# Kernel tuning notes

Measured on AMD Instinct MI355X. Metric: run time of the kernel, lower is better.

## Reference

```python
import jax, jax.numpy as jnp
import numpy as np

TEMP = 0.07
EPS = 1e-6

B = 8192
D1 = 129  # d+1 ambient Lorentz coords


def setup_inputs() -> dict:
    key = jax.random.key(0)
    k1, k2 = jax.random.split(key)
    z1 = jax.random.normal(k1, (B, D1), dtype=jnp.float32)
    z2 = jax.random.normal(k2, (B, D1), dtype=jnp.float32)
    return {"z1": z1, "z2": z2}


def _loss(z1, z2):
    # Minkowski (Lorentz) inner product via a single GEMM:
    # <x,y>_L = -x0*y0 + sum_i xi*yi  ->  x @ (metric * y)^T
    metric = jnp.concatenate([-jnp.ones((1,), z1.dtype), jnp.ones((D1 - 1,), z1.dtype)])
    inner = jnp.einsum('bd,kd->bk', z1, z2 * metric)  # (B, B)
    # Lorentz distance with curvature c=1: acosh(clamp(-<x,y>_L, 1+eps))
    dist = jnp.arccosh(jnp.clip(-inner, 1.0 + EPS, None))
    sims = -dist / TEMP
    # symmetric InfoNCE: labels are the diagonal
    logp_t2i = jax.nn.log_softmax(sims, axis=-1)      # text -> image
    logp_i2t = jax.nn.log_softmax(sims.T, axis=-1)    # image -> text
    diag = jnp.arange(sims.shape[0])
    loss_t2i = -jnp.mean(logp_t2i[diag, diag])
    loss_i2t = -jnp.mean(logp_i2t[diag, diag])
    return (loss_t2i + loss_i2t) / 2.0


def reference(z1, z2):
    return _loss(z1, z2)
```

## Files before the change

### kernel.cpp

```cpp
#include <hip/hip_runtime.h>
#include <math.h>


#define BDIM   8192
#define K_IN   129
#define K_PAD  160
#define BK     32
#define NKT    (K_PAD / BK)
#define CTILES 4

typedef __bf16  bf16x8 __attribute__((ext_vector_type(8)));
typedef float   f32x4  __attribute__((ext_vector_type(4)));

#define OFF_A    0u
#define OFF_B    (BDIM * K_PAD * 2u)
#define OFF_RS   (2u * BDIM * K_PAD * 2u)
#define OFF_CP   (OFF_RS + BDIM * 4u)
#define OFF_DG   (OFF_CP + 4u * BDIM * 4u)

__device__ __forceinline__ float fast_sqrt(float x) {
#if __has_builtin(__builtin_amdgcn_sqrtf)
    return __builtin_amdgcn_sqrtf(x);
#else
    return sqrtf(x);
#endif
}
__device__ __forceinline__ float fast_log2(float x) {
#if __has_builtin(__builtin_amdgcn_logf)
    return __builtin_amdgcn_logf(x);
#else
    return __log2f(x);
#endif
}
__device__ __forceinline__ float fast_exp2(float x) {
#if __has_builtin(__builtin_amdgcn_exp2f)
    return __builtin_amdgcn_exp2f(x);
#else
    extern "C" __device__ float __ocml_native_exp2_f32(float);
    return __ocml_native_exp2_f32(x);
#endif
}

__device__ __forceinline__ unsigned short f2bf_rne(float f) {
    unsigned int u = __float_as_uint(f);
    u += 0x7FFFu + ((u >> 16) & 1u);
    return (unsigned short)(u >> 16);
}

__global__ __launch_bounds__(256) void convert_kernel(
    const float* __restrict__ z1, const float* __restrict__ z2,
    unsigned short* __restrict__ A, unsigned short* __restrict__ B,
    float* __restrict__ rs_cp)
{
    int idx = blockIdx.x * 256 + threadIdx.x;
    if (idx < 5 * BDIM) rs_cp[idx] = 0.f;
    if (idx >= BDIM * K_PAD) return;
    int r = idx / K_PAD;
    int c = idx - r * K_PAD;
    float va = 0.f, vb = 0.f;
    if (c < K_IN) {
        va = z1[r * K_IN + c];
        vb = z2[r * K_IN + c];
        if (c == 0) va = -va;
    }
    A[idx] = f2bf_rne(va);
    B[idx] = f2bf_rne(vb);
}

__global__ __launch_bounds__(256, 2) void gemm_epilogue_kernel(
    const unsigned short* __restrict__ A, const unsigned short* __restrict__ B,
    float* __restrict__ row_sum, float* __restrict__ col_part,
    float* __restrict__ diag)
{
    const int t    = threadIdx.x;
    const int lane = t & 63;
    const int wave = t >> 6;
    const int quad = lane >> 4;
    const int l16  = lane & 15;

    const int strip = blockIdx.x & 63;
    const int chunk = blockIdx.x >> 6;
    const int wr      = (wave >> 1) * 64;
    const int rowBase = strip * 128 + wr;
    const int colWave = chunk * 512 + (wave & 1) * 256;

    const unsigned short* Abase = A + (rowBase + l16) * K_PAD + quad * 8;
    float* colRep = col_part + (strip & 3) * BDIM;

    float rowp[4][4] = {};

    for (int ct = 0; ct < CTILES; ++ct) {
        const int colBase = colWave + ct * 64;
        const unsigned short* Bbase = B + (colBase + l16) * K_PAD + quad * 8;

        f32x4 acc[4][4] = {};
        #pragma unroll
        for (int kt = 0; kt < NKT; ++kt) {
            bf16x8 af[4], bfr[4];
            #pragma unroll
            for (int i = 0; i < 4; ++i) {
                af[i]  = *(const bf16x8*)(Abase + i * 16 * K_PAD + kt * BK);
                bfr[i] = *(const bf16x8*)(Bbase + i * 16 * K_PAD + kt * BK);
            }
            #pragma unroll
            for (int i = 0; i < 4; ++i)
                #pragma unroll
                for (int j = 0; j < 4; ++j)
                    acc[i][j] = __builtin_amdgcn_mfma_f32_16x16x32_bf16(
                                    af[i], bfr[j], acc[i][j], 0, 0, 0);
        }

        const bool diagTile = (colBase == rowBase);
        float colp[4] = {0.f, 0.f, 0.f, 0.f};

        #pragma unroll
        for (int i = 0; i < 4; ++i) {
            #pragma unroll
            for (int j = 0; j < 4; ++j) {
                #pragma unroll
                for (int reg = 0; reg < 4; ++reg) {
                    float inner = acc[i][j][reg];
                    float x = fmaxf(-inner, 1.000001f);
                    float s = fast_sqrt(__builtin_fmaf(x, x, -1.0f));
                    float l2u = fast_log2(x + s);
                    float e = fast_exp2(-14.285714285714286f * l2u);
                    rowp[i][reg] += e;
                    colp[j]      += e;
                    if (diagTile && i == j && (quad * 4 + reg) == l16) {
                        int R = rowBase + i * 16 + quad * 4 + reg;
                        diag[R] = -9.902102579427789f * l2u;
                    }
                }
            }
        }

        #pragma unroll
        for (int j = 0; j < 4; ++j) {
            float v = colp[j];
            v += __shfl_xor(v, 16);
            v += __shfl_xor(v, 32);
            if (quad == 0)
                atomicAdd(&colRep[colBase + j * 16 + l16], v);
        }
    }

    #pragma unroll
    for (int i = 0; i < 4; ++i) {
        #pragma unroll
        for (int reg = 0; reg < 4; ++reg) {
            float v = rowp[i][reg];
            v += __shfl_xor(v, 1);
            v += __shfl_xor(v, 2);
            v += __shfl_xor(v, 4);
            v += __shfl_xor(v, 8);
            if (l16 == 0)
                atomicAdd(&row_sum[rowBase + i * 16 + quad * 4 + reg], v);
        }
    }
}

__global__ __launch_bounds__(1024) void finalize_kernel(
    const float* __restrict__ rs, const float* __restrict__ cp,
    const float* __restrict__ dg, float* __restrict__ out)
{
    __shared__ float part[16];
    int t = threadIdx.x;
    float a = 0.f;
    const float LN2_HALF = 0.34657359027997264f;
    for (int b = t; b < BDIM; b += 1024) {
        float cs = cp[b] + cp[b + BDIM] + cp[b + 2 * BDIM] + cp[b + 3 * BDIM];
        a += LN2_HALF * (fast_log2(rs[b]) + fast_log2(cs)) - dg[b];
    }
    #pragma unroll
    for (int m = 1; m < 64; m <<= 1) a += __shfl_xor(a, m);
    if ((t & 63) == 0) part[t >> 6] = a;
    __syncthreads();
    if (t < 16) {
        float v = part[t];
        #pragma unroll
        for (int m = 1; m < 16; m <<= 1) v += __shfl_xor(v, m);
        if (t == 0) out[0] = v * (1.0f / (float)BDIM);
    }
}

extern "C" void kernel_launch(void* const* d_in, const int* in_sizes, int n_in,
                              void* d_out, int out_size, void* d_ws, size_t ws_size,
                              hipStream_t stream)
{
    const float* z1 = (const float*)d_in[0];
    const float* z2 = (const float*)d_in[1];
    float* out = (float*)d_out;

    char* ws = (char*)d_ws;
    unsigned short* A  = (unsigned short*)(ws + OFF_A);
    unsigned short* B  = (unsigned short*)(ws + OFF_B);
    float* row_sum     = (float*)(ws + OFF_RS);
    float* col_part    = (float*)(ws + OFF_CP);
    float* diag        = (float*)(ws + OFF_DG);

    convert_kernel<<<(BDIM * K_PAD + 255) / 256, 256, 0, stream>>>(
        z1, z2, A, B, row_sum );

    gemm_epilogue_kernel<<<1024, 256, 0, stream>>>(
        A, B, row_sum, col_part, diag);

    finalize_kernel<<<1, 1024, 0, stream>>>(row_sum, col_part, diag, out);
}
```

Measured before the change: 119.2 us.

## Software-pipeline GEMM loads, fuse finalize via last-block counter, vectorize convert

The GEMM loop is flattened across column tiles and k-steps, with a three-slot register buffer that issues operand loads two steps ahead so memory latency overlaps the MFMAs. The separate finalize kernel is removed: each block bumps a global counter, and the last block to finish reads the row, column and diagonal sums with atomic loads and writes the loss. The convert kernel now handles four elements per thread with vector stores, and it also zeroes the diagonal buffer and the counter. The costs are higher register pressure from the prefetch buffers and correctness that relies on the waitcnt-plus-counter ordering between blocks.

```diff
diff --git a/kernel.cpp b/kernel.cpp
--- a/kernel.cpp
+++ b/kernel.cpp
@@ -8,6 +8,9 @@
 #define BK     32
 #define NKT    (K_PAD / BK)
 #define CTILES 4
+#define NSTEP  (CTILES * NKT)
+#define NBLK   1024
+#define KQ     (K_PAD / 4)
 
 typedef __bf16  bf16x8 __attribute__((ext_vector_type(8)));
 typedef float   f32x4  __attribute__((ext_vector_type(4)));
@@ -17,6 +20,7 @@
 #define OFF_RS   (2u * BDIM * K_PAD * 2u)
 #define OFF_CP   (OFF_RS + BDIM * 4u)
 #define OFF_DG   (OFF_CP + 4u * BDIM * 4u)
+#define OFF_CNT  (OFF_DG + BDIM * 4u)
 
 __device__ __forceinline__ float fast_sqrt(float x) {
 #if __has_builtin(__builtin_amdgcn_sqrtf)
@@ -50,27 +54,39 @@
 __global__ __launch_bounds__(256) void convert_kernel(
     const float* __restrict__ z1, const float* __restrict__ z2,
     unsigned short* __restrict__ A, unsigned short* __restrict__ B,
-    float* __restrict__ rs_cp)
+    float* __restrict__ zero6, unsigned int* __restrict__ cnt)
 {
     int idx = blockIdx.x * 256 + threadIdx.x;
-    if (idx < 5 * BDIM) rs_cp[idx] = 0.f;
-    if (idx >= BDIM * K_PAD) return;
-    int r = idx / K_PAD;
-    int c = idx - r * K_PAD;
-    float va = 0.f, vb = 0.f;
-    if (c < K_IN) {
-        va = z1[r * K_IN + c];
-        vb = z2[r * K_IN + c];
-        if (c == 0) va = -va;
-    }
-    A[idx] = f2bf_rne(va);
-    B[idx] = f2bf_rne(vb);
+    if (idx == 0) *cnt = 0u;
+    if (idx < 6 * BDIM) zero6[idx] = 0.f;
+    if (idx >= BDIM * KQ) return;
+    int r = idx / KQ;
+    int k = (idx - r * KQ) * 4;
+    float va[4], vb[4];
+    #pragma unroll
+    for (int u = 0; u < 4; ++u) {
+        int c = k + u;
+        va[u] = 0.f; vb[u] = 0.f;
+        if (c < K_IN) {
+            va[u] = z1[r * K_IN + c];
+            vb[u] = z2[r * K_IN + c];
+            if (c == 0) va[u] = -va[u];
+        }
+    }
+    ushort4 ha, hb;
+    ha.x = f2bf_rne(va[0]); ha.y = f2bf_rne(va[1]);
+    ha.z = f2bf_rne(va[2]); ha.w = f2bf_rne(va[3]);
+    hb.x = f2bf_rne(vb[0]); hb.y = f2bf_rne(vb[1]);
+    hb.z = f2bf_rne(vb[2]); hb.w = f2bf_rne(vb[3]);
+    *(ushort4*)&A[r * K_PAD + k] = ha;
+    *(ushort4*)&B[r * K_PAD + k] = hb;
 }
 
 __global__ __launch_bounds__(256, 2) void gemm_epilogue_kernel(
     const unsigned short* __restrict__ A, const unsigned short* __restrict__ B,
     float* __restrict__ row_sum, float* __restrict__ col_part,
-    float* __restrict__ diag)
+    float* __restrict__ diag, unsigned int* __restrict__ cnt,
+    float* __restrict__ out)
 {
     const int t    = threadIdx.x;
     const int lane = t & 63;
@@ -84,63 +100,81 @@
     const int rowBase = strip * 128 + wr;
     const int colWave = chunk * 512 + (wave & 1) * 256;
 
-    const unsigned short* Abase = A + (rowBase + l16) * K_PAD + quad * 8;
+    const unsigned short* Ab = A + (rowBase + l16) * K_PAD + quad * 8;
+    const unsigned short* Bb = B + (colWave + l16) * K_PAD + quad * 8;
     float* colRep = col_part + (strip & 3) * BDIM;
 
     float rowp[4][4] = {};
-
-    for (int ct = 0; ct < CTILES; ++ct) {
-        const int colBase = colWave + ct * 64;
-        const unsigned short* Bbase = B + (colBase + l16) * K_PAD + quad * 8;
-
-        f32x4 acc[4][4] = {};
-        #pragma unroll
-        for (int kt = 0; kt < NKT; ++kt) {
-            bf16x8 af[4], bfr[4];
+    f32x4 acc[4][4] = {};
+    bf16x8 afb[3][4], bfb[3][4];
+
+    #pragma unroll
+    for (int s = 0; s < 2; ++s) {
+        const int ct = s / NKT, kt = s % NKT;
+        #pragma unroll
+        for (int i = 0; i < 4; ++i) {
+            afb[s][i] = *(const bf16x8*)(Ab + i * 16 * K_PAD + kt * BK);
+            bfb[s][i] = *(const bf16x8*)(Bb + (ct * 64 + i * 16) * K_PAD + kt * BK);
+        }
+    }
+
+    #pragma unroll
+    for (int s = 0; s < NSTEP; ++s) {
+        if (s + 2 < NSTEP) {
+            const int s2 = s + 2, ct2 = s2 / NKT, kt2 = s2 % NKT, sl2 = s2 % 3;
             #pragma unroll
             for (int i = 0; i < 4; ++i) {
-                af[i]  = *(const bf16x8*)(Abase + i * 16 * K_PAD + kt * BK);
-                bfr[i] = *(const bf16x8*)(Bbase + i * 16 * K_PAD + kt * BK);
+                afb[sl2][i] = *(const bf16x8*)(Ab + i * 16 * K_PAD + kt2 * BK);
+                bfb[sl2][i] = *(const bf16x8*)(Bb + (ct2 * 64 + i * 16) * K_PAD + kt2 * BK);
+            }
+        }
+        const int slot = s % 3;
+        #pragma unroll
+        for (int i = 0; i < 4; ++i)
+            #pragma unroll
+            for (int j = 0; j < 4; ++j)
+                acc[i][j] = __builtin_amdgcn_mfma_f32_16x16x32_bf16(
+                                afb[slot][i], bfb[slot][j], acc[i][j], 0, 0, 0);
+
+        if (s % NKT == NKT - 1) {
+            const int ct = s / NKT;
+            const int colBase = colWave + ct * 64;
+            const bool diagTile = (colBase == rowBase);
+            float colp[4] = {0.f, 0.f, 0.f, 0.f};
+
+            #pragma unroll
+            for (int i = 0; i < 4; ++i) {
+                #pragma unroll
+                for (int j = 0; j < 4; ++j) {
+                    #pragma unroll
+                    for (int reg = 0; reg < 4; ++reg) {
+                        float inner = acc[i][j][reg];
+                        float x = fmaxf(-inner, 1.000001f);
+                        float sq = fast_sqrt(__builtin_fmaf(x, x, -1.0f));
+                        float l2u = fast_log2(x + sq);
+                        float e = fast_exp2(-14.285714285714286f * l2u);
+                        rowp[i][reg] += e;
+                        colp[j]      += e;
+                        if (diagTile && i == j && (quad * 4 + reg) == l16) {
+                            int R = rowBase + i * 16 + quad * 4 + reg;
+                            atomicAdd(&diag[R], -9.902102579427789f * l2u);
+                        }
+                    }
+                }
+            }
+            #pragma unroll
+            for (int j = 0; j < 4; ++j) {
+                float v = colp[j];
+                v += __shfl_xor(v, 16);
+                v += __shfl_xor(v, 32);
+                if (quad == 0)
+                    atomicAdd(&colRep[colBase + j * 16 + l16], v);
             }
             #pragma unroll
             for (int i = 0; i < 4; ++i)
                 #pragma unroll
                 for (int j = 0; j < 4; ++j)
-                    acc[i][j] = __builtin_amdgcn_mfma_f32_16x16x32_bf16(
-                                    af[i], bfr[j], acc[i][j], 0, 0, 0);
-        }
-
-        const bool diagTile = (colBase == rowBase);
-        float colp[4] = {0.f, 0.f, 0.f, 0.f};
-
-        #pragma unroll
-        for (int i = 0; i < 4; ++i) {
-            #pragma unroll
-            for (int j = 0; j < 4; ++j) {
-                #pragma unroll
-                for (int reg = 0; reg < 4; ++reg) {
-                    float inner = acc[i][j][reg];
-                    float x = fmaxf(-inner, 1.000001f);
-                    float s = fast_sqrt(__builtin_fmaf(x, x, -1.0f));
-                    float l2u = fast_log2(x + s);
-                    float e = fast_exp2(-14.285714285714286f * l2u);
-                    rowp[i][reg] += e;
-                    colp[j]      += e;
-                    if (diagTile && i == j && (quad * 4 + reg) == l16) {
-                        int R = rowBase + i * 16 + quad * 4 + reg;
-                        diag[R] = -9.902102579427789f * l2u;
-                    }
-                }
-            }
-        }
-
-        #pragma unroll
-        for (int j = 0; j < 4; ++j) {
-            float v = colp[j];
-            v += __shfl_xor(v, 16);
-            v += __shfl_xor(v, 32);
-            if (quad == 0)
-                atomicAdd(&colRep[colBase + j * 16 + l16], v);
+                    acc[i][j] = (f32x4){0.f, 0.f, 0.f, 0.f};
         }
     }
 
@@ -157,29 +191,41 @@
                 atomicAdd(&row_sum[rowBase + i * 16 + quad * 4 + reg], v);
         }
     }
-}
-
-__global__ __launch_bounds__(1024) void finalize_kernel(
-    const float* __restrict__ rs, const float* __restrict__ cp,
-    const float* __restrict__ dg, float* __restrict__ out)
-{
-    __shared__ float part[16];
-    int t = threadIdx.x;
-    float a = 0.f;
-    const float LN2_HALF = 0.34657359027997264f;
-    for (int b = t; b < BDIM; b += 1024) {
-        float cs = cp[b] + cp[b + BDIM] + cp[b + 2 * BDIM] + cp[b + 3 * BDIM];
-        a += LN2_HALF * (fast_log2(rs[b]) + fast_log2(cs)) - dg[b];
-    }
-    #pragma unroll
-    for (int m = 1; m < 64; m <<= 1) a += __shfl_xor(a, m);
-    if ((t & 63) == 0) part[t >> 6] = a;
+
+    __builtin_amdgcn_s_waitcnt(0);
+    __shared__ unsigned int lastFlag;
+    __shared__ float part[4];
     __syncthreads();
-    if (t < 16) {
-        float v = part[t];
-        #pragma unroll
-        for (int m = 1; m < 16; m <<= 1) v += __shfl_xor(v, m);
-        if (t == 0) out[0] = v * (1.0f / (float)BDIM);
+    if (t == 0) {
+        unsigned int old = atomicAdd(cnt, 1u);
+        lastFlag = (old == NBLK - 1u) ? 1u : 0u;
+    }
+    __syncthreads();
+    if (lastFlag) {
+        const float LN2_HALF = 0.34657359027997264f;
+        float a = 0.f;
+        for (int b = t; b < BDIM; b += 256) {
+            float r = __hip_atomic_load(&row_sum[b], __ATOMIC_RELAXED,
+                                        __HIP_MEMORY_SCOPE_AGENT);
+            float c0 = __hip_atomic_load(&col_part[b], __ATOMIC_RELAXED,
+                                         __HIP_MEMORY_SCOPE_AGENT);
+            float c1 = __hip_atomic_load(&col_part[b + BDIM], __ATOMIC_RELAXED,
+                                         __HIP_MEMORY_SCOPE_AGENT);
+            float c2 = __hip_atomic_load(&col_part[b + 2 * BDIM], __ATOMIC_RELAXED,
+                                         __HIP_MEMORY_SCOPE_AGENT);
+            float c3 = __hip_atomic_load(&col_part[b + 3 * BDIM], __ATOMIC_RELAXED,
+                                         __HIP_MEMORY_SCOPE_AGENT);
+            float d = __hip_atomic_load(&diag[b], __ATOMIC_RELAXED,
+                                        __HIP_MEMORY_SCOPE_AGENT);
+            a += LN2_HALF * (fast_log2(r) + fast_log2(c0 + c1 + c2 + c3)) - d;
+        }
+        #pragma unroll
+        for (int m = 1; m < 64; m <<= 1) a += __shfl_xor(a, m);
+        if (lane == 0) part[wave] = a;
+        __syncthreads();
+        if (t == 0)
+            out[0] = (part[0] + part[1] + part[2] + part[3])
+                     * (1.0f / (float)BDIM);
     }
 }
 
@@ -197,12 +243,11 @@
     float* row_sum     = (float*)(ws + OFF_RS);
     float* col_part    = (float*)(ws + OFF_CP);
     float* diag        = (float*)(ws + OFF_DG);
-
-    convert_kernel<<<(BDIM * K_PAD + 255) / 256, 256, 0, stream>>>(
-        z1, z2, A, B, row_sum );
-
-    gemm_epilogue_kernel<<<1024, 256, 0, stream>>>(
-        A, B, row_sum, col_part, diag);
-
-    finalize_kernel<<<1, 1024, 0, stream>>>(row_sum, col_part, diag, out);
-}
+    unsigned int* cnt  = (unsigned int*)(ws + OFF_CNT);
+
+    convert_kernel<<<(BDIM * KQ + 255) / 256, 256, 0, stream>>>(
+        z1, z2, A, B, row_sum , cnt);
+
+    gemm_epilogue_kernel<<<NBLK, 256, 0, stream>>>(
+        A, B, row_sum, col_part, diag, cnt, out);
+}
```

Measured after the change: 164.1 us. 1.38x slower.
